# Kernel optimization log

Hardware: AMD Instinct MI355X
Metric: run time of the kernel (lower is better)

Reference implementation:

```python
import jax, jax.numpy as jnp
import numpy as np

NL, D, H, MLP, P, HW, L, KEEP = 6, 1024, 16, 4096, 16, 14, 196, 98
DH = D // H


def layer_norm(x, s, b):
    m = jnp.mean(x, axis=-1, keepdims=True)
    v = jnp.mean(jnp.square(x - m), axis=-1, keepdims=True)
    return (x - m) * jax.lax.rsqrt(v + 1e-6) * s + b


def gather_by_einsum(x, ids):
    # faithful to FLIP: one-hot gather expressed as matmul (sharding-friendly)
    mat = jax.nn.one_hot(ids, x.shape[1], dtype=x.dtype)
    return jnp.einsum('nl...,nkl->nk...', x, mat)


def setup_inputs():
    key = jax.random.key(0)
    ks = jax.random.split(key, 10)
    s = 0.02
    return {
        'imgs': jax.random.normal(ks[0], (32, 224, 224, 3), jnp.float32),
        'noise': jax.random.uniform(ks[1], (32, L), jnp.float32),
        'patch_w': jax.random.normal(ks[2], (P * P * 3, D), jnp.float32) * s,
        'patch_b': jnp.zeros((D,), jnp.float32),
        'pos_emb': jax.random.normal(ks[3], (1, L, D), jnp.float32) * s,
        'cls_token': jnp.zeros((1, 1, D), jnp.float32),
        'ln1_s': jnp.ones((NL, D), jnp.float32),
        'ln1_b': jnp.zeros((NL, D), jnp.float32),
        'wq': jax.random.normal(ks[4], (NL, D, D), jnp.float32) * s,
        'bq': jnp.zeros((NL, D), jnp.float32),
        'wk': jax.random.normal(ks[5], (NL, D, D), jnp.float32) * s,
        'bk': jnp.zeros((NL, D), jnp.float32),
        'wv': jax.random.normal(ks[6], (NL, D, D), jnp.float32) * s,
        'bv': jnp.zeros((NL, D), jnp.float32),
        'wo': jax.random.normal(ks[7], (NL, D, D), jnp.float32) * s,
        'bo': jnp.zeros((NL, D), jnp.float32),
        'ln2_s': jnp.ones((NL, D), jnp.float32),
        'ln2_b': jnp.zeros((NL, D), jnp.float32),
        'w1': jax.random.normal(ks[8], (NL, D, MLP), jnp.float32) * s,
        'b1': jnp.zeros((NL, MLP), jnp.float32),
        'w2': jax.random.normal(ks[9], (NL, MLP, D), jnp.float32) * s,
        'b2': jnp.zeros((NL, D), jnp.float32),
        'lnf_s': jnp.ones((D,), jnp.float32),
        'lnf_b': jnp.zeros((D,), jnp.float32),
    }


def reference(imgs, noise, patch_w, patch_b, pos_emb, cls_token,
              ln1_s, ln1_b, wq, bq, wk, bk, wv, bv, wo, bo,
              ln2_s, ln2_b, w1, b1, w2, b2, lnf_s, lnf_b):
    N = imgs.shape[0]
    # patchify: (N,224,224,3) -> (N, L=196, 768); stride-16 conv == patch matmul
    x = imgs.reshape(N, HW, P, HW, P, 3).transpose(0, 1, 3, 2, 4, 5).reshape(N, L, P * P * 3)
    x = x @ patch_w + patch_b          # (N, L, D)
    x = x + pos_emb

    # random_mask (mask_ratio=0.5 -> keep 98 of 196 tokens)
    ids_shuffle = jnp.argsort(noise, axis=1)
    ids_restore = jnp.argsort(ids_shuffle, axis=1)
    ids_keep = ids_shuffle[:, :KEEP]
    x = gather_by_einsum(x, ids_keep)  # (N, KEEP, D)
    mask = jnp.ones((N, L), x.dtype).at[:, :KEEP].set(0.0)
    mask = gather_by_einsum(mask, ids_restore)  # (N, L)

    # prepend cls token -> (N, 1+KEEP, D)
    x = jnp.concatenate([jnp.tile(cls_token, (N, 1, 1)), x], axis=1)

    scale = 1.0 / np.sqrt(DH).astype(np.float32)
    S = x.shape[1]
    for i in range(NL):
        y = layer_norm(x, ln1_s[i], ln1_b[i])
        q = (y @ wq[i] + bq[i]).reshape(N, S, H, DH)
        k = (y @ wk[i] + bk[i]).reshape(N, S, H, DH)
        v = (y @ wv[i] + bv[i]).reshape(N, S, H, DH)
        att = jax.nn.softmax(jnp.einsum('nqhd,nkhd->nhqk', q, k) * scale, axis=-1)
        o = jnp.einsum('nhqk,nkhd->nqhd', att, v).reshape(N, S, D)
        x = x + o @ wo[i] + bo[i]
        y = layer_norm(x, ln2_s[i], ln2_b[i])
        y = jax.nn.gelu(y @ w1[i] + b1[i]) @ w2[i] + b2[i]
        x = x + y
    x = layer_norm(x, lnf_s, lnf_b)
    return x, mask
```

## Files before the change

### kernel.cpp

```cpp
#include <hip/hip_runtime.h>
#include <hip/hip_bf16.h>
#include <math.h>

#define NLAYERS 6
#define DMODEL  1024
#define NHEADS  16
#define DHEAD   64
#define DMLP    4096
#define PSZ     16
#define HWN     14
#define LTOK    196
#define NKEEP   98
#define NIMG    32
#define SEQ     99
#define NS      (NIMG * SEQ)
#define NP      (NIMG * LTOK)
#define PDIM    768
#define QS      3072
#define SPAD    112
#define VT_PITCH 136
#define P_PITCH  136

typedef __attribute__((ext_vector_type(8))) short short8;
typedef __attribute__((ext_vector_type(4))) float f32x4;

__device__ __forceinline__ void gload16(const void* g, void* l) {
    __builtin_amdgcn_global_load_lds(
        (const __attribute__((address_space(1))) void*)g,
        (__attribute__((address_space(3))) void*)l, 16, 0, 0);
}

__global__ __launch_bounds__(256) void conv_transpose(
    const float* __restrict__ W, __hip_bfloat16* __restrict__ Wt, int K, int N,
    size_t src_zs, size_t dst_zs)
{
    __shared__ float tile[32][33];
    W += (size_t)blockIdx.z * src_zs;
    Wt += (size_t)blockIdx.z * dst_zs;
    int n0 = blockIdx.x * 32, k0 = blockIdx.y * 32;
    int tx = threadIdx.x & 31, ty = threadIdx.x >> 5;
#pragma unroll
    for (int i = 0; i < 4; ++i)
        tile[ty + i * 8][tx] = W[(size_t)(k0 + ty + i * 8) * N + n0 + tx];
    __syncthreads();
#pragma unroll
    for (int i = 0; i < 4; ++i)
        Wt[(size_t)(n0 + ty + i * 8) * K + k0 + tx] = __float2bfloat16(tile[tx][ty + i * 8]);
}

__global__ __launch_bounds__(256) void concat_bias(
    const float* __restrict__ bq, const float* __restrict__ bk,
    const float* __restrict__ bv, float* __restrict__ bqkv)
{
    int L = blockIdx.y;
    int i = blockIdx.x * 256 + threadIdx.x;
    float v;
    if (i < DMODEL)            v = bq[L * DMODEL + i];
    else if (i < 2 * DMODEL)   v = bk[L * DMODEL + i - DMODEL];
    else                       v = bv[L * DMODEL + i - 2 * DMODEL];
    bqkv[(size_t)L * QS + i] = v;
}

__global__ __launch_bounds__(256) void sort_kernel(
    const float* __restrict__ noise, int* __restrict__ ids_keep, float* __restrict__ mask)
{
    int n = blockIdx.x, tid = threadIdx.x;
    __shared__ float nz[LTOK];
    if (tid < LTOK) nz[tid] = noise[n * LTOK + tid];
    __syncthreads();
    if (tid < LTOK) {
        float val = nz[tid];
        int rank = 0;
        for (int j = 0; j < LTOK; ++j) {
            float vj = nz[j];
            rank += (vj < val) || (vj == val && j < tid);
        }
        mask[n * LTOK + tid] = (rank < NKEEP) ? 0.0f : 1.0f;
        if (rank < NKEEP) ids_keep[n * NKEEP + rank] = tid;
    }
}

__global__ __launch_bounds__(256) void patchify(
    const float* __restrict__ imgs, __hip_bfloat16* __restrict__ Ap)
{
    int row = blockIdx.x, tid = threadIdx.x;
    int n = row / LTOK, l = row % LTOK;
    int hy = l / HWN, hx = l % HWN;
    int py = tid >> 4, px = tid & 15;
    const float* src = imgs + (((size_t)(n * 224 + hy * 16 + py)) * 224 + hx * 16 + px) * 3;
    __hip_bfloat16* dst = Ap + (size_t)row * PDIM + tid * 3;
    dst[0] = __float2bfloat16(src[0]);
    dst[1] = __float2bfloat16(src[1]);
    dst[2] = __float2bfloat16(src[2]);
}

__global__ __launch_bounds__(256) void gather_cls(
    const float* __restrict__ x0, const float* __restrict__ cls,
    const int* __restrict__ ids_keep, float* __restrict__ x)
{
    int row = blockIdx.x, tid = threadIdx.x;
    int n = row / SEQ, s = row % SEQ;
    const float* src = (s == 0) ? cls
        : x0 + ((size_t)n * LTOK + ids_keep[n * NKEEP + (s - 1)]) * DMODEL;
    reinterpret_cast<float4*>(x + (size_t)row * DMODEL)[tid] =
        reinterpret_cast<const float4*>(src)[tid];
}

template <int OUTMODE>
__global__ __launch_bounds__(256) void ln_kernel(
    const float* __restrict__ x, const float* __restrict__ s, const float* __restrict__ b,
    float* __restrict__ of, __hip_bfloat16* __restrict__ ob)
{
    int row = blockIdx.x, tid = threadIdx.x;
    int lane = tid & 63, wid = tid >> 6;
    float4 t = reinterpret_cast<const float4*>(x + (size_t)row * DMODEL)[tid];
    float sum = t.x + t.y + t.z + t.w;
    float sq  = t.x * t.x + t.y * t.y + t.z * t.z + t.w * t.w;
#pragma unroll
    for (int m = 1; m < 64; m <<= 1) { sum += __shfl_xor(sum, m); sq += __shfl_xor(sq, m); }
    __shared__ float sm[8];
    if (lane == 0) { sm[wid] = sum; sm[4 + wid] = sq; }
    __syncthreads();
    sum = sm[0] + sm[1] + sm[2] + sm[3];
    sq  = sm[4] + sm[5] + sm[6] + sm[7];
    float mean = sum * (1.0f / DMODEL);
    float var  = sq * (1.0f / DMODEL) - mean * mean;
    float rstd = rsqrtf(var + 1e-6f);
    float4 sv = reinterpret_cast<const float4*>(s)[tid];
    float4 bv = reinterpret_cast<const float4*>(b)[tid];
    float o0 = (t.x - mean) * rstd * sv.x + bv.x;
    float o1 = (t.y - mean) * rstd * sv.y + bv.y;
    float o2 = (t.z - mean) * rstd * sv.z + bv.z;
    float o3 = (t.w - mean) * rstd * sv.w + bv.w;
    if (OUTMODE == 0) {
        reinterpret_cast<float4*>(of + (size_t)row * DMODEL)[tid] = make_float4(o0, o1, o2, o3);
    } else {
        __hip_bfloat16* p = ob + (size_t)row * DMODEL + tid * 4;
        p[0] = __float2bfloat16(o0); p[1] = __float2bfloat16(o1);
        p[2] = __float2bfloat16(o2); p[3] = __float2bfloat16(o3);
    }
}

template <int MODE>
__global__ __launch_bounds__(256) void gemm_mfma(
    const __hip_bfloat16* __restrict__ A, const __hip_bfloat16* __restrict__ Wt,
    const float* __restrict__ bias, const float* __restrict__ pos,
    float* __restrict__ Cf, __hip_bfloat16* __restrict__ Cb,
    int M, int N, int K)
{
    __shared__ __hip_bfloat16 As[128 * 32];
    __shared__ __hip_bfloat16 Bs[128 * 32];

    int tid = threadIdx.x;
    int lane = tid & 63, wid = tid >> 6;
    int quad = lane >> 4, l16 = lane & 15;
    int wm = wid & 1, wn = wid >> 1;
    int bm = blockIdx.x * 128, bn = blockIdx.y * 128;

    int rowA0 = tid >> 2,        rowA1 = (tid + 256) >> 2;
    int kcA0 = (tid & 3) ^ ((tid >> 3) & 3);
    int kcA1 = (tid & 3) ^ (((tid + 256) >> 3) & 3);
    int arow0 = bm + rowA0; if (arow0 >= M) arow0 = M - 1;
    int arow1 = bm + rowA1; if (arow1 >= M) arow1 = M - 1;
    const short* Ag0 = reinterpret_cast<const short*>(A) + (size_t)arow0 * K + kcA0 * 8;
    const short* Ag1 = reinterpret_cast<const short*>(A) + (size_t)arow1 * K + kcA1 * 8;
    const short* Bg0 = reinterpret_cast<const short*>(Wt) + (size_t)(bn + rowA0) * K + kcA0 * 8;
    const short* Bg1 = reinterpret_cast<const short*>(Wt) + (size_t)(bn + rowA1) * K + kcA1 * 8;
    char* AsDst0 = (char*)As + tid * 16;
    char* AsDst1 = (char*)As + (tid + 256) * 16;
    char* BsDst0 = (char*)Bs + tid * 16;
    char* BsDst1 = (char*)Bs + (tid + 256) * 16;

    int aOff[4], bOff[4];
#pragma unroll
    for (int t = 0; t < 4; ++t) {
        int row = wm * 64 + t * 16 + l16;
        aOff[t] = row * 64 + (quad ^ ((row >> 1) & 3)) * 16;
        int col = wn * 64 + t * 16 + l16;
        bOff[t] = col * 64 + (quad ^ ((col >> 1) & 3)) * 16;
    }

    f32x4 acc[4][4];
#pragma unroll
    for (int t = 0; t < 4; ++t)
#pragma unroll
        for (int u = 0; u < 4; ++u) { f32x4 z = {0.f, 0.f, 0.f, 0.f}; acc[t][u] = z; }

    for (int k0 = 0; k0 < K; k0 += 32) {
        gload16(Ag0 + k0, AsDst0);
        gload16(Ag1 + k0, AsDst1);
        gload16(Bg0 + k0, BsDst0);
        gload16(Bg1 + k0, BsDst1);
        __syncthreads();

        short8 a[4], b[4];
#pragma unroll
        for (int t = 0; t < 4; ++t) a[t] = *reinterpret_cast<const short8*>((char*)As + aOff[t]);
#pragma unroll
        for (int u = 0; u < 4; ++u) b[u] = *reinterpret_cast<const short8*>((char*)Bs + bOff[u]);
#pragma unroll
        for (int t = 0; t < 4; ++t)
#pragma unroll
            for (int u = 0; u < 4; ++u)
                acc[t][u] = __builtin_amdgcn_mfma_f32_16x16x32_bf16(a[t], b[u], acc[t][u], 0, 0, 0);
        __syncthreads();
    }

#pragma unroll
    for (int t = 0; t < 4; ++t) {
#pragma unroll
        for (int u = 0; u < 4; ++u) {
            int col = bn + wn * 64 + u * 16 + l16;
            float bcol = bias ? bias[col] : 0.0f;
#pragma unroll
            for (int i = 0; i < 4; ++i) {
                int row = bm + wm * 64 + t * 16 + quad * 4 + i;
                if (row >= M) continue;
                float val = acc[t][u][i] + bcol;
                size_t idx = (size_t)row * N + col;
                if (MODE == 0) {
                    if (pos) val += pos[(size_t)(row % LTOK) * N + col];
                    Cf[idx] = val;
                } else if (MODE == 1) {
                    Cf[idx] += val;
                } else if (MODE == 2) {
                    float u3 = val * val * val;
                    float g = 0.5f * val *
                        (1.0f + tanhf(0.7978845608028654f * (val + 0.044715f * u3)));
                    Cb[idx] = __float2bfloat16(g);
                } else {
                    Cb[idx] = __float2bfloat16(val);
                }
            }
        }
    }
}

__global__ __launch_bounds__(256) void attn_mfma(
    const __hip_bfloat16* __restrict__ qkv, __hip_bfloat16* __restrict__ o)
{
    int n = blockIdx.x >> 4, h = blockIdx.x & 15;
    int tid = threadIdx.x, lane = tid & 63, wid = tid >> 6;
    int quad = lane >> 4, l16 = lane & 15;

    __shared__ __hip_bfloat16 Vt[DHEAD * VT_PITCH];
    __shared__ __hip_bfloat16 Ps[4][16 * P_PITCH];

    {
        int4 zz = make_int4(0, 0, 0, 0);
        int4* v4 = (int4*)Vt;
        int4* p4 = (int4*)Ps;
        for (int i = tid; i < (DHEAD * VT_PITCH) / 8; i += 256) v4[i] = zz;
        for (int i = tid; i < (4 * 16 * P_PITCH) / 8; i += 256) p4[i] = zz;
    }
    __syncthreads();
    for (int idx = tid; idx < SEQ * DHEAD; idx += 256) {
        int s = idx >> 6, d = idx & 63;
        Vt[d * VT_PITCH + s] = qkv[((size_t)(n * SEQ + s)) * QS + 2 * DMODEL + h * DHEAD + d];
    }
    __syncthreads();

    const short* qbase = reinterpret_cast<const short*>(qkv) + (size_t)n * SEQ * QS + h * DHEAD;
    const short* kbase = qbase + DMODEL;
    const float scale = 0.125f;

    for (int qt = wid; qt < 7; qt += 4) {
        int q0 = qt * 16;
        int qrow = q0 + l16; if (qrow >= SEQ) qrow = SEQ - 1;
        const short* qp = qbase + (size_t)qrow * QS + quad * 8;
        short8 aq0 = *reinterpret_cast<const short8*>(qp);
        short8 aq1 = *reinterpret_cast<const short8*>(qp + 32);

        f32x4 sc[7];
#pragma unroll
        for (int u = 0; u < 7; ++u) {
            int krow = u * 16 + l16; if (krow >= SEQ) krow = SEQ - 1;
            const short* kp = kbase + (size_t)krow * QS + quad * 8;
            short8 kb0 = *reinterpret_cast<const short8*>(kp);
            short8 kb1 = *reinterpret_cast<const short8*>(kp + 32);
            f32x4 s = {0.f, 0.f, 0.f, 0.f};
            s = __builtin_amdgcn_mfma_f32_16x16x32_bf16(aq0, kb0, s, 0, 0, 0);
            s = __builtin_amdgcn_mfma_f32_16x16x32_bf16(aq1, kb1, s, 0, 0, 0);
            sc[u] = s;
        }
#pragma unroll
        for (int u = 0; u < 7; ++u)
#pragma unroll
            for (int i = 0; i < 4; ++i)
                sc[u][i] *= scale;
        if (l16 >= 3) {
#pragma unroll
            for (int i = 0; i < 4; ++i) sc[6][i] = -1e30f;
        }
#pragma unroll
        for (int i = 0; i < 4; ++i) {
            float m = sc[0][i];
#pragma unroll
            for (int u = 1; u < 7; ++u) m = fmaxf(m, sc[u][i]);
            m = fmaxf(m, __shfl_xor(m, 1));
            m = fmaxf(m, __shfl_xor(m, 2));
            m = fmaxf(m, __shfl_xor(m, 4));
            m = fmaxf(m, __shfl_xor(m, 8));
            float sum = 0.f;
#pragma unroll
            for (int u = 0; u < 7; ++u) {
                float e = __expf(sc[u][i] - m);
                sc[u][i] = e;
                sum += e;
            }
            sum += __shfl_xor(sum, 1);
            sum += __shfl_xor(sum, 2);
            sum += __shfl_xor(sum, 4);
            sum += __shfl_xor(sum, 8);
            float inv = 1.0f / sum;
            __hip_bfloat16* pr = &Ps[wid][(quad * 4 + i) * P_PITCH];
#pragma unroll
            for (int u = 0; u < 7; ++u)
                pr[u * 16 + l16] = __float2bfloat16(sc[u][i] * inv);
        }
        short8 ap[4];
#pragma unroll
        for (int kc = 0; kc < 4; ++kc)
            ap[kc] = *reinterpret_cast<const short8*>(&Ps[wid][l16 * P_PITCH + kc * 32 + quad * 8]);
        f32x4 oacc[4];
#pragma unroll
        for (int dt = 0; dt < 4; ++dt) { f32x4 z = {0.f, 0.f, 0.f, 0.f}; oacc[dt] = z; }
#pragma unroll
        for (int kc = 0; kc < 4; ++kc) {
#pragma unroll
            for (int dt = 0; dt < 4; ++dt) {
                short8 vb = *reinterpret_cast<const short8*>(
                    &Vt[(dt * 16 + l16) * VT_PITCH + kc * 32 + quad * 8]);
                oacc[dt] = __builtin_amdgcn_mfma_f32_16x16x32_bf16(ap[kc], vb, oacc[dt], 0, 0, 0);
            }
        }
#pragma unroll
        for (int dt = 0; dt < 4; ++dt) {
#pragma unroll
            for (int i = 0; i < 4; ++i) {
                int row = q0 + quad * 4 + i;
                if (row < SEQ)
                    o[((size_t)(n * SEQ + row)) * DMODEL + h * DHEAD + dt * 16 + l16] =
                        __float2bfloat16(oacc[dt][i]);
            }
        }
    }
}

extern "C" void kernel_launch(void* const* d_in, const int* in_sizes, int n_in,
                              void* d_out, int out_size, void* d_ws, size_t ws_size,
                              hipStream_t stream)
{
    (void)in_sizes; (void)n_in; (void)out_size; (void)ws_size;
    const float* imgs    = (const float*)d_in[0];
    const float* noise   = (const float*)d_in[1];
    const float* patch_w = (const float*)d_in[2];
    const float* patch_b = (const float*)d_in[3];
    const float* pos_emb = (const float*)d_in[4];
    const float* cls     = (const float*)d_in[5];
    const float* ln1_s   = (const float*)d_in[6];
    const float* ln1_b   = (const float*)d_in[7];
    const float* wq      = (const float*)d_in[8];
    const float* bq      = (const float*)d_in[9];
    const float* wk      = (const float*)d_in[10];
    const float* bk      = (const float*)d_in[11];
    const float* wv      = (const float*)d_in[12];
    const float* bv      = (const float*)d_in[13];
    const float* wo      = (const float*)d_in[14];
    const float* bo      = (const float*)d_in[15];
    const float* ln2_s   = (const float*)d_in[16];
    const float* ln2_b   = (const float*)d_in[17];
    const float* w1      = (const float*)d_in[18];
    const float* b1      = (const float*)d_in[19];
    const float* w2      = (const float*)d_in[20];
    const float* b2      = (const float*)d_in[21];
    const float* lnf_s   = (const float*)d_in[22];
    const float* lnf_b   = (const float*)d_in[23];

    float* out_x    = (float*)d_out;
    float* out_mask = out_x + (size_t)NS * DMODEL;

    char* p = (char*)d_ws;
    auto alloc = [&](size_t bytes) {
        char* r = p; p += (bytes + 255) & ~(size_t)255; return r;
    };
    __hip_bfloat16* patch_wt = (__hip_bfloat16*)alloc((size_t)DMODEL * PDIM * 2);
    __hip_bfloat16* wqkvt    = (__hip_bfloat16*)alloc((size_t)NLAYERS * QS * DMODEL * 2);
    __hip_bfloat16* wot = (__hip_bfloat16*)alloc((size_t)NLAYERS * DMODEL * DMODEL * 2);
    __hip_bfloat16* w1t = (__hip_bfloat16*)alloc((size_t)NLAYERS * DMODEL * DMLP * 2);
    __hip_bfloat16* w2t = (__hip_bfloat16*)alloc((size_t)NLAYERS * DMODEL * DMLP * 2);
    float* bqkv     = (float*)alloc((size_t)NLAYERS * QS * 4);
    int*   ids_keep = (int*)alloc((size_t)NIMG * NKEEP * 4);
    float* x        = (float*)alloc((size_t)NS * DMODEL * 4);
    char* scratch = p;
    __hip_bfloat16* ybf  = (__hip_bfloat16*)alloc((size_t)NS * DMODEL * 2);
    __hip_bfloat16* qkv  = (__hip_bfloat16*)alloc((size_t)NS * QS * 2);
    __hip_bfloat16* obf  = (__hip_bfloat16*)alloc((size_t)NS * DMODEL * 2);
    __hip_bfloat16* h1bf = (__hip_bfloat16*)alloc((size_t)NS * DMLP * 2);
    __hip_bfloat16* Apatch = (__hip_bfloat16*)scratch;
    float* x0 = (float*)(scratch + (((size_t)NP * PDIM * 2 + 255) & ~(size_t)255));

    const size_t DD = (size_t)DMODEL * DMODEL;
    const size_t DM = (size_t)DMODEL * DMLP;

    conv_transpose<<<dim3(DMODEL / 32, PDIM / 32, 1), 256, 0, stream>>>(
        patch_w, patch_wt, PDIM, DMODEL, PDIM * DMODEL, PDIM * DMODEL);
    conv_transpose<<<dim3(DMODEL / 32, DMODEL / 32, NLAYERS), 256, 0, stream>>>(
        wq, wqkvt, DMODEL, DMODEL, DD, (size_t)QS * DMODEL);
    conv_transpose<<<dim3(DMODEL / 32, DMODEL / 32, NLAYERS), 256, 0, stream>>>(
        wk, wqkvt + DD, DMODEL, DMODEL, DD, (size_t)QS * DMODEL);
    conv_transpose<<<dim3(DMODEL / 32, DMODEL / 32, NLAYERS), 256, 0, stream>>>(
        wv, wqkvt + 2 * DD, DMODEL, DMODEL, DD, (size_t)QS * DMODEL);
    conv_transpose<<<dim3(DMODEL / 32, DMODEL / 32, NLAYERS), 256, 0, stream>>>(
        wo, wot, DMODEL, DMODEL, DD, DD);
    conv_transpose<<<dim3(DMLP / 32, DMODEL / 32, NLAYERS), 256, 0, stream>>>(
        w1, w1t, DMODEL, DMLP, DM, DM);
    conv_transpose<<<dim3(DMODEL / 32, DMLP / 32, NLAYERS), 256, 0, stream>>>(
        w2, w2t, DMLP, DMODEL, DM, DM);
    concat_bias<<<dim3(QS / 256, NLAYERS), 256, 0, stream>>>(bq, bk, bv, bqkv);

    sort_kernel<<<NIMG, 256, 0, stream>>>(noise, ids_keep, out_mask);
    patchify<<<NP, 256, 0, stream>>>(imgs, Apatch);
    gemm_mfma<0><<<dim3(NP / 128, DMODEL / 128), 256, 0, stream>>>(
        Apatch, patch_wt, patch_b, pos_emb, x0, nullptr, NP, DMODEL, PDIM);
    gather_cls<<<NS, 256, 0, stream>>>(x0, cls, ids_keep, x);

    dim3 gQKV((NS + 127) / 128, QS / 128);
    dim3 gD((NS + 127) / 128, DMODEL / 128);
    dim3 gM((NS + 127) / 128, DMLP / 128);
    for (int L = 0; L < NLAYERS; ++L) {
        size_t wDD = (size_t)L * DD;
        size_t wDM = (size_t)L * DM;
        ln_kernel<1><<<NS, 256, 0, stream>>>(x, ln1_s + L * DMODEL, ln1_b + L * DMODEL, nullptr, ybf);
        gemm_mfma<3><<<gQKV, 256, 0, stream>>>(ybf, wqkvt + (size_t)L * QS * DMODEL,
                                               bqkv + (size_t)L * QS, nullptr, nullptr, qkv,
                                               NS, QS, DMODEL);
        attn_mfma<<<NIMG * NHEADS, 256, 0, stream>>>(qkv, obf);
        gemm_mfma<1><<<gD, 256, 0, stream>>>(obf, wot + wDD, bo + L * DMODEL, nullptr, x, nullptr, NS, DMODEL, DMODEL);
        ln_kernel<1><<<NS, 256, 0, stream>>>(x, ln2_s + L * DMODEL, ln2_b + L * DMODEL, nullptr, ybf);
        gemm_mfma<2><<<gM, 256, 0, stream>>>(ybf, w1t + wDM, b1 + L * DMLP, nullptr, nullptr, h1bf, NS, DMLP, DMODEL);
        gemm_mfma<1><<<gD, 256, 0, stream>>>(h1bf, w2t + wDM, b2 + L * DMODEL, nullptr, x, nullptr, NS, DMODEL, DMLP);
    }

    ln_kernel<0><<<NS, 256, 0, stream>>>(x, lnf_s, lnf_b, out_x, nullptr);
}
```

Baseline: 2.269 ms.

## Double-buffer GEMM shared tiles and split-K residual GEMMs with atomic accumulation

The GEMM kernel now keeps two shared-memory buffers, so the global load of the next K tile is issued while MFMA runs on the current one, and each K step needs one barrier instead of two. The residual-add GEMMs (Wo and W2) also split K across gridDim.z (2 and 4 ways) and accumulate into x with atomicAdd. Only the z=0 slice adds the bias. This raises occupancy for the small 25x8 grids, at the cost of atomic traffic, doubled LDS use and non-deterministic summation order.

```diff
diff --git a/kernel.cpp b/kernel.cpp
--- a/kernel.cpp
+++ b/kernel.cpp
@@ -148,28 +148,26 @@
     float* __restrict__ Cf, __hip_bfloat16* __restrict__ Cb,
     int M, int N, int K)
 {
-    __shared__ __hip_bfloat16 As[128 * 32];
-    __shared__ __hip_bfloat16 Bs[128 * 32];
+    __shared__ __hip_bfloat16 As[2][128 * 32];
+    __shared__ __hip_bfloat16 Bs[2][128 * 32];
 
     int tid = threadIdx.x;
     int lane = tid & 63, wid = tid >> 6;
     int quad = lane >> 4, l16 = lane & 15;
     int wm = wid & 1, wn = wid >> 1;
     int bm = blockIdx.x * 128, bn = blockIdx.y * 128;
+    int Kc = K / gridDim.z;
+    int koff = blockIdx.z * Kc;
 
     int rowA0 = tid >> 2,        rowA1 = (tid + 256) >> 2;
     int kcA0 = (tid & 3) ^ ((tid >> 3) & 3);
     int kcA1 = (tid & 3) ^ (((tid + 256) >> 3) & 3);
     int arow0 = bm + rowA0; if (arow0 >= M) arow0 = M - 1;
     int arow1 = bm + rowA1; if (arow1 >= M) arow1 = M - 1;
-    const short* Ag0 = reinterpret_cast<const short*>(A) + (size_t)arow0 * K + kcA0 * 8;
-    const short* Ag1 = reinterpret_cast<const short*>(A) + (size_t)arow1 * K + kcA1 * 8;
-    const short* Bg0 = reinterpret_cast<const short*>(Wt) + (size_t)(bn + rowA0) * K + kcA0 * 8;
-    const short* Bg1 = reinterpret_cast<const short*>(Wt) + (size_t)(bn + rowA1) * K + kcA1 * 8;
-    char* AsDst0 = (char*)As + tid * 16;
-    char* AsDst1 = (char*)As + (tid + 256) * 16;
-    char* BsDst0 = (char*)Bs + tid * 16;
-    char* BsDst1 = (char*)Bs + (tid + 256) * 16;
+    const short* Ag0 = reinterpret_cast<const short*>(A) + (size_t)arow0 * K + koff + kcA0 * 8;
+    const short* Ag1 = reinterpret_cast<const short*>(A) + (size_t)arow1 * K + koff + kcA1 * 8;
+    const short* Bg0 = reinterpret_cast<const short*>(Wt) + (size_t)(bn + rowA0) * K + koff + kcA0 * 8;
+    const short* Bg1 = reinterpret_cast<const short*>(Wt) + (size_t)(bn + rowA1) * K + koff + kcA1 * 8;
 
     int aOff[4], bOff[4];
 #pragma unroll
@@ -186,32 +184,47 @@
 #pragma unroll
         for (int u = 0; u < 4; ++u) { f32x4 z = {0.f, 0.f, 0.f, 0.f}; acc[t][u] = z; }
 
-    for (int k0 = 0; k0 < K; k0 += 32) {
-        gload16(Ag0 + k0, AsDst0);
-        gload16(Ag1 + k0, AsDst1);
-        gload16(Bg0 + k0, BsDst0);
-        gload16(Bg1 + k0, BsDst1);
-        __syncthreads();
-
+    auto stage = [&](int buf, int k0) {
+        char* ad = (char*)As[buf];
+        char* bd = (char*)Bs[buf];
+        gload16(Ag0 + k0, ad + tid * 16);
+        gload16(Ag1 + k0, ad + (tid + 256) * 16);
+        gload16(Bg0 + k0, bd + tid * 16);
+        gload16(Bg1 + k0, bd + (tid + 256) * 16);
+    };
+    auto compute = [&](int buf) {
+        const char* ab = (const char*)As[buf];
+        const char* bb = (const char*)Bs[buf];
         short8 a[4], b[4];
 #pragma unroll
-        for (int t = 0; t < 4; ++t) a[t] = *reinterpret_cast<const short8*>((char*)As + aOff[t]);
-#pragma unroll
-        for (int u = 0; u < 4; ++u) b[u] = *reinterpret_cast<const short8*>((char*)Bs + bOff[u]);
+        for (int t = 0; t < 4; ++t) a[t] = *reinterpret_cast<const short8*>(ab + aOff[t]);
+#pragma unroll
+        for (int u = 0; u < 4; ++u) b[u] = *reinterpret_cast<const short8*>(bb + bOff[u]);
 #pragma unroll
         for (int t = 0; t < 4; ++t)
 #pragma unroll
             for (int u = 0; u < 4; ++u)
                 acc[t][u] = __builtin_amdgcn_mfma_f32_16x16x32_bf16(a[t], b[u], acc[t][u], 0, 0, 0);
+    };
+
+    stage(0, 0);
+    __syncthreads();
+    for (int k0 = 0; k0 < Kc; k0 += 64) {
+        stage(1, k0 + 32);
+        compute(0);
         __syncthreads();
-    }
-
+        if (k0 + 64 < Kc) stage(0, k0 + 64);
+        compute(1);
+        __syncthreads();
+    }
+
+    bool addb = (bias != nullptr) && (blockIdx.z == 0);
 #pragma unroll
     for (int t = 0; t < 4; ++t) {
 #pragma unroll
         for (int u = 0; u < 4; ++u) {
             int col = bn + wn * 64 + u * 16 + l16;
-            float bcol = bias ? bias[col] : 0.0f;
+            float bcol = addb ? bias[col] : 0.0f;
 #pragma unroll
             for (int i = 0; i < 4; ++i) {
                 int row = bm + wm * 64 + t * 16 + quad * 4 + i;
@@ -222,7 +235,7 @@
                     if (pos) val += pos[(size_t)(row % LTOK) * N + col];
                     Cf[idx] = val;
                 } else if (MODE == 1) {
-                    Cf[idx] += val;
+                    atomicAdd(&Cf[idx], val);
                 } else if (MODE == 2) {
                     float u3 = val * val * val;
                     float g = 0.5f * val *
@@ -428,6 +441,8 @@
     dim3 gQKV((NS + 127) / 128, QS / 128);
     dim3 gD((NS + 127) / 128, DMODEL / 128);
     dim3 gM((NS + 127) / 128, DMLP / 128);
+    dim3 gWo((NS + 127) / 128, DMODEL / 128, 2);
+    dim3 gW2((NS + 127) / 128, DMODEL / 128, 4);
     for (int L = 0; L < NLAYERS; ++L) {
         size_t wDD = (size_t)L * DD;
         size_t wDM = (size_t)L * DM;
@@ -436,10 +451,10 @@
                                                bqkv + (size_t)L * QS, nullptr, nullptr, qkv,
                                                NS, QS, DMODEL);
         attn_mfma<<<NIMG * NHEADS, 256, 0, stream>>>(qkv, obf);
-        gemm_mfma<1><<<gD, 256, 0, stream>>>(obf, wot + wDD, bo + L * DMODEL, nullptr, x, nullptr, NS, DMODEL, DMODEL);
+        gemm_mfma<1><<<gWo, 256, 0, stream>>>(obf, wot + wDD, bo + L * DMODEL, nullptr, x, nullptr, NS, DMODEL, DMODEL);
         ln_kernel<1><<<NS, 256, 0, stream>>>(x, ln2_s + L * DMODEL, ln2_b + L * DMODEL, nullptr, ybf);
         gemm_mfma<2><<<gM, 256, 0, stream>>>(ybf, w1t + wDM, b1 + L * DMLP, nullptr, nullptr, h1bf, NS, DMLP, DMODEL);
-        gemm_mfma<1><<<gD, 256, 0, stream>>>(h1bf, w2t + wDM, b2 + L * DMODEL, nullptr, x, nullptr, NS, DMODEL, DMLP);
+        gemm_mfma<1><<<gW2, 256, 0, stream>>>(h1bf, w2t + wDM, b2 + L * DMODEL, nullptr, x, nullptr, NS, DMODEL, DMLP);
     }
 
     ln_kernel<0><<<NS, 256, 0, stream>>>(x, lnf_s, lnf_b, out_x, nullptr);
```

New measurement: 2.266 ms. No clear change (-0.1%).
